# Optimization experiments

Measured on AMD Instinct MI355X. Metric: run time of the kernel, lower is better.

Reference implementation:

```python
import jax, jax.numpy as jnp
import numpy as np

DEPTH, DIM, HEADS, DH = 2, 1024, 16, 64
B, N, MEM, TEXT = 8, 256, 4, 64
PH, PW, PS = 4, 4, 16
EXP_H, EXP_W, EXP_T = 4, 4, 2
RH, RW, RT = 2*EXP_H+1, 2*EXP_W+1, 2*EXP_T+1  # 9,9,5
CUR_IDX = 20
MEM_IDXS = [0, 5, 10, 15]
SCALE = DH ** -0.5


def _pos(idx):
    # get_pos_from_idx_down_right
    nf = PH * PW
    inner = idx % nf
    return inner % PH, inner // PH, idx // nf


def _axial_freqs():
    # 2D axial rotary freqs over the (PH*PS)x(PW*PS) pixel grid, rot_dim = DH
    GH, GW = PH * PS, PW * PS
    nfa = DH // 4  # 16 base freqs per axis -> 32 dims per axis after pair-repeat
    inv = 1.0 / (10000.0 ** (np.arange(nfa, dtype=np.float64) / nfa))
    fh = np.repeat(np.arange(GH)[:, None] * inv[None, :], 2, axis=-1)  # [GH,32]
    fw = np.repeat(np.arange(GW)[:, None] * inv[None, :], 2, axis=-1)  # [GW,32]
    return np.concatenate([
        np.broadcast_to(fh[:, None, :], (GH, GW, DH // 2)),
        np.broadcast_to(fw[None, :, :], (GH, GW, DH // 2)),
    ], axis=-1).astype(np.float32)  # [GH,GW,DH]


def setup_inputs() -> dict:
    key = jax.random.key(0)
    ks = jax.random.split(key, 14)
    p = lambda k, shape: jax.random.normal(k, shape, jnp.float32) * 0.02
    x = jax.random.normal(ks[0], (B, N, DIM), jnp.float32)
    cond = jax.random.normal(ks[1], (B, MEM * N + TEXT, DIM), jnp.float32)
    Wq = p(ks[2], (DEPTH, DIM, HEADS * DH))
    Wk = p(ks[3], (DEPTH, DIM, HEADS * DH))
    Wv = p(ks[4], (DEPTH, DIM, HEADS * DH))
    Wo = p(ks[5], (DEPTH, HEADS * DH, DIM))
    bo = jnp.zeros((DEPTH, DIM), jnp.float32)
    rpe = p(ks[6], (DEPTH, RH * RW * RT, HEADS))
    W1 = p(ks[7], (DEPTH, DIM, DIM * 4 * 2))
    b1 = jnp.zeros((DEPTH, DIM * 8), jnp.float32)
    W2 = p(ks[8], (DEPTH, DIM * 4, DIM))
    b2 = jnp.zeros((DEPTH, DIM), jnp.float32)
    freqs = _axial_freqs()
    def block(idx):
        r, c, _ = _pos(idx)
        return freqs[r * PS:(r + 1) * PS, c * PS:(c + 1) * PS].reshape(-1, DH)
    src_freq = jnp.asarray(block(CUR_IDX))
    tgt_freq = jnp.asarray(np.concatenate([block(i) for i in MEM_IDXS], axis=0))
    sr, sc, st = _pos(CUR_IDX)
    rel = [(tr - sr + EXP_H) * RW + (tc - sc + EXP_W) + (tt - st + EXP_T) * RH * RW
           for (tr, tc, tt) in map(_pos, MEM_IDXS)]
    rel_idx = jnp.asarray(rel, jnp.int32)
    return dict(x=x, cond=cond, Wq=Wq, Wk=Wk, Wv=Wv, Wo=Wo, bo=bo, rpe=rpe,
                W1=W1, b1=b1, W2=W2, b2=b2, src_freq=src_freq, tgt_freq=tgt_freq,
                rel_idx=rel_idx)


def _rotate_half(t):
    # pairs interleaved: (d r) with r=2
    tr = t.reshape(t.shape[:-1] + (-1, 2))
    t1, t2 = tr[..., 0], tr[..., 1]
    return jnp.stack((-t2, t1), axis=-1).reshape(t.shape)


def _apply_rotary(freqs, t):
    return t * jnp.cos(freqs) + _rotate_half(t) * jnp.sin(freqs)


def reference(x, cond, Wq, Wk, Wv, Wo, bo, rpe, W1, b1, W2, b2, src_freq, tgt_freq, rel_idx):
    MS = MEM * N  # memory token count in cond
    split_heads = lambda t: t.reshape(t.shape[0], t.shape[1], HEADS, DH).transpose(0, 2, 1, 3)
    for l in range(DEPTH):
        # --- FullCrossAttention ---
        q = split_heads(x @ Wq[l])          # [b,h,n,dh]
        k = split_heads(cond @ Wk[l])       # [b,h,j,dh]
        v = split_heads(cond @ Wv[l])
        # gathered relative-position bias added to k (broadcast over feature dim)
        bias = rpe[l][rel_idx]              # [mem, h]
        bias_k = jnp.repeat(bias.T, N, axis=1)[None, :, :, None]  # [1,h,mem*S,1]
        k = k.at[:, :, :MS, :].add(bias_k)
        # inline rotary: src freqs on q, gathered target freqs on memory keys
        q = _apply_rotary(src_freq, q)
        k = k.at[:, :, :MS, :].set(_apply_rotary(tgt_freq, k[:, :, :MS, :]))
        dots = jnp.einsum('bhid,bhjd->bhij', q, k) * SCALE
        attn = jax.nn.softmax(dots, axis=-1)
        out = jnp.einsum('bhij,bhjd->bhid', attn, v)
        out = out.transpose(0, 2, 1, 3).reshape(x.shape[0], N, HEADS * DH)
        x = x + out @ Wo[l] + bo[l]
        # --- GEGLU FeedForward ---
        hgl = x @ W1[l] + b1[l]
        a, g = jnp.split(hgl, 2, axis=-1)
        y = a * jax.nn.gelu(g, approximate=False)
        x = x + y @ W2[l] + b2[l]
    return x
```

## Files before the change

kernel.cpp:

```cpp
#include <hip/hip_runtime.h>
#include <hip/hip_bf16.h>
#include <math.h>

typedef __hip_bfloat16 bf16;
typedef __bf16 bf16x8 __attribute__((ext_vector_type(8)));
typedef float f32x4 __attribute__((ext_vector_type(4)));

typedef __attribute__((address_space(3))) void lds_void;
typedef const __attribute__((address_space(1))) void gbl_void;

__device__ __forceinline__ float b2f(bf16 v) { return __bfloat162float(v); }
__device__ __forceinline__ bf16 f2b(float v) { return __float2bfloat16(v); }

__device__ __forceinline__ f32x4 shfl_xor4(f32x4 v, int m) {
  f32x4 o;
  o[0] = __shfl_xor(v[0], m);
  o[1] = __shfl_xor(v[1], m);
  o[2] = __shfl_xor(v[2], m);
  o[3] = __shfl_xor(v[3], m);
  return o;
}
__device__ __forceinline__ f32x4 max4(f32x4 a, f32x4 b) {
  f32x4 o;
  o[0] = fmaxf(a[0], b[0]); o[1] = fmaxf(a[1], b[1]);
  o[2] = fmaxf(a[2], b[2]); o[3] = fmaxf(a[3], b[3]);
  return o;
}
__device__ __forceinline__ f32x4 exp4(f32x4 a) {
  f32x4 o;
  o[0] = __expf(a[0]); o[1] = __expf(a[1]);
  o[2] = __expf(a[2]); o[3] = __expf(a[3]);
  return o;
}

__device__ __forceinline__ void cbar(int ahead) {
  if (ahead >= 2)      asm volatile("s_waitcnt vmcnt(8)" ::: "memory");
  else if (ahead == 1) asm volatile("s_waitcnt vmcnt(4)" ::: "memory");
  else                 asm volatile("s_waitcnt vmcnt(0)" ::: "memory");
  __builtin_amdgcn_s_barrier();
  __builtin_amdgcn_sched_barrier(0);
}
__device__ __forceinline__ void cbar2(int ahead) {
  if (ahead >= 1) asm volatile("s_waitcnt vmcnt(4)" ::: "memory");
  else            asm volatile("s_waitcnt vmcnt(0)" ::: "memory");
  __builtin_amdgcn_s_barrier();
  __builtin_amdgcn_sched_barrier(0);
}

__device__ __forceinline__ int xcd_swz(int flat, int nwg) {
  int q = nwg >> 3, r = nwg & 7;
  int xcd = flat & 7, pos = flat >> 3;
  return (xcd < r) ? (xcd * (q + 1) + pos) : (r * (q + 1) + (xcd - r) * q + pos);
}

__global__ void detect_dtype(const unsigned int* __restrict__ x, int* __restrict__ flag) {
  int cnt = 0;
  for (int i = 0; i < 128; ++i) {
    unsigned int lo = x[i] & 0xFFFFu;
    unsigned int e = (lo >> 7) & 0xFFu;
    if (e >= 100u && e <= 140u) ++cnt;
  }
  *flag = (cnt >= 96) ? 1 : 0;
}

__global__ void convert_in(const void* __restrict__ src, bf16* __restrict__ dst,
                           int n, const int* __restrict__ flag) {
  int i = blockIdx.x * 256 + threadIdx.x;
  if (i >= n) return;
  dst[i] = (*flag) ? ((const bf16*)src)[i] : f2b(((const float*)src)[i]);
}

__global__ void emit_kernel(const float* __restrict__ xf, const int* __restrict__ flag,
                            void* __restrict__ out) {
  int i = blockIdx.x * 256 + threadIdx.x;
  if (*flag) ((bf16*)out)[i] = f2b(xf[i]);
  else       ((float*)out)[i] = xf[i];
}

template<int HALF>
__device__ __forceinline__ bf16x8 frag_ld(const __bf16* lt, int r, int quad) {
  constexpr int LB = (HALF == 128) ? 7 : 6;
  int line = r & (HALF - 1);
  int sl = (((r >> LB) << 2) | quad) ^ (line & 7);
  return *(const bf16x8*)&lt[line * 64 + sl * 8];
}

template<int TAG>
__global__ __launch_bounds__(256, 3) void gemm_bt(
    const bf16* __restrict__ A, int lda,
    const bf16* __restrict__ Bt, int ldb,
    float alpha,
    const float* __restrict__ resid,
    const bf16* __restrict__ bias,
    float* __restrict__ outf,
    bf16* __restrict__ outb,
    int ldc, int K)
{
  __shared__ char smem[49152] __attribute__((aligned(16)));
  float* lC = (float*)smem;

  int tid = threadIdx.x;
  int lane = tid & 63;
  int wave = tid >> 6;
  int quad = lane >> 4, l16 = lane & 15;
  int wm = (wave >> 1) * 64, wn = (wave & 1) * 64;

  int gx = gridDim.x, gy = gridDim.y;
  int nwg = gx * gy;
  bool ymaj = gy >= gx;
  int flat = ymaj ? ((int)blockIdx.y * gx + blockIdx.x)
                  : ((int)blockIdx.x * gy + blockIdx.y);
  int swz = xcd_swz(flat, nwg);
  int bx, by;
  if (ymaj) { by = swz / gx; bx = swz - by * gx; }
  else      { bx = swz / gy; by = swz - bx * gy; }
  int row0 = by * 128, col0 = bx * 128;

  const bf16* asrc[2]; const bf16* bsrc[2];
#pragma unroll
  for (int i = 0; i < 2; ++i) {
    int line = i * 32 + (tid >> 3);
    int hx = (tid & 7) ^ (line & 7);
    int r = line + ((hx >> 2) << 6);
    int ke = (hx & 3) << 3;
    asrc[i] = A + (long long)(row0 + r) * lda + ke;
    bsrc[i] = Bt + (long long)(col0 + r) * ldb + ke;
  }

  auto stage = [&](int b, int t) {
    int o = t * 32;
#pragma unroll
    for (int i = 0; i < 2; ++i) {
      __builtin_amdgcn_global_load_lds((gbl_void*)(asrc[i] + o),
          (lds_void*)(smem + b * 8192 + i * 4096 + wave * 1024), 16, 0, 0);
      __builtin_amdgcn_global_load_lds((gbl_void*)(bsrc[i] + o),
          (lds_void*)(smem + 24576 + b * 8192 + i * 4096 + wave * 1024), 16, 0, 0);
    }
  };

  f32x4 acc[4][4];
#pragma unroll
  for (int a = 0; a < 4; ++a)
#pragma unroll
    for (int b = 0; b < 4; ++b) acc[a][b] = (f32x4){0.f, 0.f, 0.f, 0.f};

  int nk = K >> 5;
  stage(0, 0); stage(1, 1);
  cbar2(1);

  for (int t = 0; t < nk; ++t) {
    if (t + 2 < nk) stage((t + 2) % 3, t + 2);
    int bt = t % 3;
    const __bf16* lA = (const __bf16*)(smem + bt * 8192);
    const __bf16* lB = (const __bf16*)(smem + 24576 + bt * 8192);
    bf16x8 af[4], bfr[4];
#pragma unroll
    for (int mi = 0; mi < 4; ++mi) af[mi] = frag_ld<64>(lA, wm + mi * 16 + l16, quad);
#pragma unroll
    for (int ni = 0; ni < 4; ++ni) bfr[ni] = frag_ld<64>(lB, wn + ni * 16 + l16, quad);
    __builtin_amdgcn_s_setprio(1);
#pragma unroll
    for (int mi = 0; mi < 4; ++mi)
#pragma unroll
      for (int ni = 0; ni < 4; ++ni)
        acc[mi][ni] = __builtin_amdgcn_mfma_f32_16x16x32_bf16(
            af[mi], bfr[ni], acc[mi][ni], 0, 0, 0);
    __builtin_amdgcn_s_setprio(0);
    int ahead = nk - 1 - (t + 1); if (ahead > 1) ahead = 1;
    cbar2(ahead);
  }

#pragma unroll
  for (int half = 0; half < 2; ++half) {
    __syncthreads();
    if ((wave >> 1) == half) {
#pragma unroll
      for (int mi = 0; mi < 4; ++mi)
#pragma unroll
        for (int ni = 0; ni < 4; ++ni)
#pragma unroll
          for (int r = 0; r < 4; ++r)
            lC[(mi * 16 + quad * 4 + r) * 128 + wn + ni * 16 + l16] =
                acc[mi][ni][r] * alpha;
    }
    __syncthreads();
#pragma unroll
    for (int i = 0; i < 8; ++i) {
      int f = i * 256 + tid;
      int row = f >> 5, cc = (f & 31) * 4;
      int m = row0 + half * 64 + row, n = col0 + cc;
      f32x4 v = *(const f32x4*)&lC[row * 128 + cc];
      long long ci = (long long)m * ldc + n;
      if (bias) {
        v[0] += b2f(bias[n]);     v[1] += b2f(bias[n + 1]);
        v[2] += b2f(bias[n + 2]); v[3] += b2f(bias[n + 3]);
      }
      if (resid) v += *(const f32x4*)&resid[ci];
      if (outf) *(f32x4*)&outf[ci] = v;
      if (outb) {
        bf16 c0 = f2b(v[0]), c1 = f2b(v[1]), c2 = f2b(v[2]), c3 = f2b(v[3]);
        ushort4 o = { *(unsigned short*)&c0, *(unsigned short*)&c1,
                      *(unsigned short*)&c2, *(unsigned short*)&c3 };
        *(ushort4*)&outb[ci] = o;
      }
    }
  }
}

__global__ __launch_bounds__(512, 2) void gemm256_geglu(
    const bf16* __restrict__ A, int lda,
    const bf16* __restrict__ W1t, int ldb,
    const bf16* __restrict__ bias,
    bf16* __restrict__ outy, int ldy, int K)
{
  __shared__ char smem[131072] __attribute__((aligned(16)));
  float* lC = (float*)smem;

  int tid = threadIdx.x;
  int lane = tid & 63;
  int wave = tid >> 6;
  int quad = lane >> 4, l16 = lane & 15;
  int wr = wave >> 2, wc = wave & 3;
  int wm = wr * 128, wn = wc * 64;
  int row0 = blockIdx.y * 256, col0 = blockIdx.x * 128;

  const bf16* asrc[2]; const bf16* bsrc[2];
#pragma unroll
  for (int i = 0; i < 2; ++i) {
    int line = i * 64 + (tid >> 3);
    int hx = (tid & 7) ^ (line & 7);
    int rA = line + ((hx >> 2) << 7);
    int ke = (hx & 3) << 3;
    asrc[i] = A + (long long)(row0 + rA) * lda + ke;
    int rowW = (hx & 4) ? (4096 + col0 + line) : (col0 + line);
    bsrc[i] = W1t + (long long)rowW * ldb + ke;
  }

  auto stage = [&](int b, int t) {
    int o = t * 32;
#pragma unroll
    for (int i = 0; i < 2; ++i) {
      __builtin_amdgcn_global_load_lds((gbl_void*)(asrc[i] + o),
          (lds_void*)(smem + b * 16384 + i * 8192 + wave * 1024), 16, 0, 0);
      __builtin_amdgcn_global_load_lds((gbl_void*)(bsrc[i] + o),
          (lds_void*)(smem + 65536 + b * 16384 + i * 8192 + wave * 1024), 16, 0, 0);
    }
  };

  f32x4 acc[8][4];
#pragma unroll
  for (int a = 0; a < 8; ++a)
#pragma unroll
    for (int b = 0; b < 4; ++b) acc[a][b] = (f32x4){0.f, 0.f, 0.f, 0.f};

  int nk = K >> 5;
  stage(0, 0); stage(1, 1); stage(2, 2);
  cbar(2);

  for (int t = 0; t < nk; ++t) {
    if (t + 3 < nk) stage((t + 3) & 3, t + 3);
    const __bf16* lA = (const __bf16*)(smem + (t & 3) * 16384);
    const __bf16* lB = (const __bf16*)(smem + 65536 + (t & 3) * 16384);
    bf16x8 af[8], bfr[4];
#pragma unroll
    for (int mi = 0; mi < 8; ++mi) af[mi] = frag_ld<128>(lA, wm + mi * 16 + l16, quad);
#pragma unroll
    for (int ni = 0; ni < 4; ++ni) bfr[ni] = frag_ld<128>(lB, wn + ni * 16 + l16, quad);
    __builtin_amdgcn_s_setprio(1);
#pragma unroll
    for (int mi = 0; mi < 8; ++mi)
#pragma unroll
      for (int ni = 0; ni < 4; ++ni)
        acc[mi][ni] = __builtin_amdgcn_mfma_f32_16x16x32_bf16(
            af[mi], bfr[ni], acc[mi][ni], 0, 0, 0);
    __builtin_amdgcn_s_setprio(0);
    int hi = t + 3; if (hi > nk - 1) hi = nk - 1;
    cbar(hi - (t + 1));
  }

#pragma unroll
  for (int h = 0; h < 2; ++h) {
    __syncthreads();
    if (wr == h) {
#pragma unroll
      for (int mi = 0; mi < 8; ++mi)
#pragma unroll
        for (int ni = 0; ni < 4; ++ni)
#pragma unroll
          for (int r = 0; r < 4; ++r)
            lC[(mi * 16 + quad * 4 + r) * 256 + wn + ni * 16 + l16] =
                acc[mi][ni][r];
    }
    __syncthreads();
#pragma unroll
    for (int it = 0; it < 8; ++it) {
      int f = it * 512 + tid;
      int row = f >> 5, cc = (f & 31) * 4;
      int m = row0 + h * 128 + row, n = col0 + cc;
      f32x4 a = *(const f32x4*)&lC[row * 256 + cc];
      f32x4 g = *(const f32x4*)&lC[row * 256 + 128 + cc];
      bf16 yb[4];
#pragma unroll
      for (int j = 0; j < 4; ++j) {
        float av = a[j] + b2f(bias[n + j]);
        float gv = g[j] + b2f(bias[4096 + n + j]);
        float ge = 0.5f * gv * (1.0f + erff(gv * 0.70710678118654752f));
        yb[j] = f2b(av * ge);
      }
      ushort4 o = { *(unsigned short*)&yb[0], *(unsigned short*)&yb[1],
                    *(unsigned short*)&yb[2], *(unsigned short*)&yb[3] };
      *(ushort4*)&outy[(long long)m * ldy + n] = o;
    }
  }
}

__global__ __launch_bounds__(256, 3) void gemm_splitk(
    const bf16* __restrict__ A, int lda,
    const bf16* __restrict__ Bt, int ldb,
    float* __restrict__ pbuf, int ldc, int M, int KC)
{
  __shared__ char smem[49152] __attribute__((aligned(16)));

  int koff = blockIdx.z * KC;
  float* outz = pbuf + (long long)blockIdx.z * M * ldc;
  int tid = threadIdx.x;
  int lane = tid & 63;
  int wave = tid >> 6;
  int quad = lane >> 4, l16 = lane & 15;
  int wm = (wave >> 1) * 64, wn = (wave & 1) * 64;

  int gx = gridDim.x, gy = gridDim.y;
  int nwg = gx * gy;
  bool ymaj = gy >= gx;
  int flat = ymaj ? ((int)blockIdx.y * gx + blockIdx.x)
                  : ((int)blockIdx.x * gy + blockIdx.y);
  int swz = xcd_swz(flat, nwg);
  int bx, by;
  if (ymaj) { by = swz / gx; bx = swz - by * gx; }
  else      { bx = swz / gy; by = swz - bx * gy; }
  int row0 = by * 128, col0 = bx * 128;

  const bf16* asrc[2]; const bf16* bsrc[2];
#pragma unroll
  for (int i = 0; i < 2; ++i) {
    int line = i * 32 + (tid >> 3);
    int hx = (tid & 7) ^ (line & 7);
    int r = line + ((hx >> 2) << 6);
    int ke = (hx & 3) << 3;
    asrc[i] = A + (long long)(row0 + r) * lda + koff + ke;
    bsrc[i] = Bt + (long long)(col0 + r) * ldb + koff + ke;
  }

  auto stage = [&](int b, int t) {
    int o = t * 32;
#pragma unroll
    for (int i = 0; i < 2; ++i) {
      __builtin_amdgcn_global_load_lds((gbl_void*)(asrc[i] + o),
          (lds_void*)(smem + b * 8192 + i * 4096 + wave * 1024), 16, 0, 0);
      __builtin_amdgcn_global_load_lds((gbl_void*)(bsrc[i] + o),
          (lds_void*)(smem + 24576 + b * 8192 + i * 4096 + wave * 1024), 16, 0, 0);
    }
  };

  f32x4 acc[4][4];
#pragma unroll
  for (int a = 0; a < 4; ++a)
#pragma unroll
    for (int b = 0; b < 4; ++b) acc[a][b] = (f32x4){0.f, 0.f, 0.f, 0.f};

  int nk = KC >> 5;
  stage(0, 0); stage(1, 1);
  cbar2(1);

  for (int t = 0; t < nk; ++t) {
    if (t + 2 < nk) stage((t + 2) % 3, t + 2);
    int bt = t % 3;
    const __bf16* lA = (const __bf16*)(smem + bt * 8192);
    const __bf16* lB = (const __bf16*)(smem + 24576 + bt * 8192);
    bf16x8 af[4], bfr[4];
#pragma unroll
    for (int mi = 0; mi < 4; ++mi) af[mi] = frag_ld<64>(lA, wm + mi * 16 + l16, quad);
#pragma unroll
    for (int ni = 0; ni < 4; ++ni) bfr[ni] = frag_ld<64>(lB, wn + ni * 16 + l16, quad);
    __builtin_amdgcn_s_setprio(1);
#pragma unroll
    for (int mi = 0; mi < 4; ++mi)
#pragma unroll
      for (int ni = 0; ni < 4; ++ni)
        acc[mi][ni] = __builtin_amdgcn_mfma_f32_16x16x32_bf16(
            af[mi], bfr[ni], acc[mi][ni], 0, 0, 0);
    __builtin_amdgcn_s_setprio(0);
    int ahead = nk - 1 - (t + 1); if (ahead > 1) ahead = 1;
    cbar2(ahead);
  }

#pragma unroll
  for (int mi = 0; mi < 4; ++mi)
#pragma unroll
    for (int ni = 0; ni < 4; ++ni) {
      int n = col0 + wn + ni * 16 + l16;
#pragma unroll
      for (int r = 0; r < 4; ++r) {
        int m = row0 + wm + mi * 16 + quad * 4 + r;
        outz[(long long)m * ldc + n] = acc[mi][ni][r];
      }
    }
}

__global__ void reduce_ff2(const float* __restrict__ pbuf, const bf16* __restrict__ bias,
                           float* __restrict__ xf, bf16* __restrict__ xbf) {
  int i = blockIdx.x * 256 + threadIdx.x;
  const int NT = 2048 * 1024;
  float v = xf[i] + b2f(bias[i & 1023]) +
            pbuf[i] + pbuf[i + NT] + pbuf[i + 2 * NT] + pbuf[i + 3 * NT];
  xf[i] = v;
  xbf[i] = f2b(v);
}

__device__ __forceinline__ void fa_stage(
    const bf16* __restrict__ kb, const bf16* __restrict__ vtb, int j0, int tk,
    char* smem, int kboff, int vboff, int tid, int wave)
{
  int rounds = tk >> 6;
  for (int i = 0; i < rounds; ++i) {
    int rowk = i * 64 + (tid >> 3);
    int cbk = ((tid & 7) * 16) ^ ((rowk & 7) << 4);
    __builtin_amdgcn_global_load_lds(
        (gbl_void*)(kb + (long long)(j0 + rowk) * 1024 + (cbk >> 1)),
        (lds_void*)(smem + kboff + i * 8192 + wave * 1024), 16, 0, 0);
    int rowv, cbv;
    if (tk == 128) { rowv = i * 32 + (tid >> 4); cbv = ((tid & 15) * 16) ^ ((rowv & 7) << 4); }
    else           { rowv = (tid >> 3);          cbv = ((tid & 7) * 16) ^ ((rowv & 7) << 4); }
    __builtin_amdgcn_global_load_lds(
        (gbl_void*)(vtb + (long long)rowv * 8704 + j0 + (cbv >> 1)),
        (lds_void*)(smem + vboff + i * 8192 + wave * 1024), 16, 0, 0);
  }
}

template<int TK>
__device__ __forceinline__ void fa_compute(
    const char* smem, int kboff, int vboff,
    const bf16x8 (&qa)[2], bf16* lPw,
    int quad, int l16,
    f32x4 (&accO)[4], f32x4& mrow, f32x4& lrow)
{
  constexpr int NT = TK / 16;
  constexpr int NCH = TK / 32;
  const __bf16* lK = (const __bf16*)(smem + kboff);
  const __bf16* lV = (const __bf16*)(smem + vboff);
  int xork = (l16 & 7) << 3;

  f32x4 accS[NT];
#pragma unroll
  for (int ni = 0; ni < NT; ++ni) accS[ni] = (f32x4){0.f, 0.f, 0.f, 0.f};

#pragma unroll
  for (int ni = 0; ni < NT; ++ni)
#pragma unroll
    for (int ks = 0; ks < 2; ++ks) {
      bf16x8 bfr = *(const bf16x8*)&lK[(ni * 16 + l16) * 64 + ((ks * 32 + quad * 8) ^ xork)];
      accS[ni] = __builtin_amdgcn_mfma_f32_16x16x32_bf16(qa[ks], bfr, accS[ni], 0, 0, 0);
    }

  f32x4 vmax = (f32x4){-INFINITY, -INFINITY, -INFINITY, -INFINITY};
#pragma unroll
  for (int ni = 0; ni < NT; ++ni) {
    accS[ni] *= 0.125f;
    vmax = max4(vmax, accS[ni]);
  }
#pragma unroll
  for (int m = 1; m <= 8; m <<= 1) vmax = max4(vmax, shfl_xor4(vmax, m));
  f32x4 mnew = max4(mrow, vmax);
  f32x4 alpha = exp4(mrow - mnew);
  f32x4 rs = (f32x4){0.f, 0.f, 0.f, 0.f};
#pragma unroll
  for (int ni = 0; ni < NT; ++ni) {
    accS[ni] = exp4(accS[ni] - mnew);
    rs += accS[ni];
  }
#pragma unroll
  for (int m = 1; m <= 8; m <<= 1) rs += shfl_xor4(rs, m);
  lrow = lrow * alpha + rs;
  mrow = mnew;
#pragma unroll
  for (int nd = 0; nd < 4; ++nd) accO[nd] *= alpha;

#pragma unroll
  for (int c = 0; c < NCH; ++c) {
#pragma unroll
    for (int u = 0; u < 2; ++u)
#pragma unroll
      for (int r = 0; r < 4; ++r)
        lPw[(quad * 4 + r) * 40 + u * 16 + l16] = f2b(accS[c * 2 + u][r]);
    bf16x8 pa = *(const bf16x8*)&lPw[l16 * 40 + quad * 8];
#pragma unroll
    for (int nd = 0; nd < 4; ++nd) {
      bf16x8 vb = *(const bf16x8*)&lV[(nd * 16 + l16) * TK + ((c * 32 + quad * 8) ^ xork)];
      accO[nd] = __builtin_amdgcn_mfma_f32_16x16x32_bf16(pa, vb, accO[nd], 0, 0, 0);
    }
  }
}

__global__ __launch_bounds__(512, 2) void flash_attn(
    const bf16* __restrict__ q, const bf16* __restrict__ k,
    const bf16* __restrict__ vt, bf16* __restrict__ att)
{
  __shared__ char smem[75776] __attribute__((aligned(16)));

  int idx = xcd_swz(blockIdx.x, gridDim.x);
  int b = idx >> 5, h = (idx >> 1) & 15, half = idx & 1;
  int tid = threadIdx.x, wave = tid >> 6, lane = tid & 63;
  int quad = lane >> 4, l16 = lane & 15;
  int qrow0 = b * 256 + half * 128 + wave * 16;

  const bf16* kb  = k  + (long long)b * 1088 * 1024 + h * 64;
  const bf16* vtb = vt + (long long)(h * 64) * 8704 + b * 1088;
  bf16* lPw = (bf16*)(smem + 65536 + wave * 1280);

  bf16x8 qa[2];
#pragma unroll
  for (int ks = 0; ks < 2; ++ks)
    qa[ks] = *(const bf16x8*)&q[(long long)(qrow0 + l16) * 1024 +
                                h * 64 + ks * 32 + quad * 8];

  f32x4 accO[4];
  f32x4 mrow = (f32x4){-INFINITY, -INFINITY, -INFINITY, -INFINITY};
  f32x4 lrow = (f32x4){0.f, 0.f, 0.f, 0.f};
#pragma unroll
  for (int nd = 0; nd < 4; ++nd) accO[nd] = (f32x4){0.f, 0.f, 0.f, 0.f};

  fa_stage(kb, vtb, 0, 128, smem, 0, 32768, tid, wave);
  __syncthreads();

  for (int jt = 0; jt < 8; ++jt) {
    int buf = (jt & 1) * 16384;
    int nbuf = 16384 - buf;
    if (jt < 7) fa_stage(kb, vtb, (jt + 1) * 128, 128, smem, nbuf, 32768 + nbuf, tid, wave);
    else        fa_stage(kb, vtb, 1024, 64, smem, nbuf, 32768 + nbuf, tid, wave);
    fa_compute<128>(smem, buf, 32768 + buf, qa, lPw, quad, l16, accO, mrow, lrow);
    __syncthreads();
  }
  fa_compute<64>(smem, 0, 32768, qa, lPw, quad, l16, accO, mrow, lrow);

  f32x4 inv;
  inv[0] = 1.f / lrow[0]; inv[1] = 1.f / lrow[1];
  inv[2] = 1.f / lrow[2]; inv[3] = 1.f / lrow[3];
#pragma unroll
  for (int nd = 0; nd < 4; ++nd) {
    f32x4 o = accO[nd] * inv;
#pragma unroll
    for (int r = 0; r < 4; ++r)
      att[(long long)(qrow0 + quad * 4 + r) * 1024 +
          h * 64 + nd * 16 + l16] = f2b(o[r]);
  }
}

__global__ void init_x_kernel(const void* __restrict__ x, const int* __restrict__ flag,
                              float* __restrict__ xf, bf16* __restrict__ xbf) {
  int i = blockIdx.x * 256 + threadIdx.x;
  float v = (*flag) ? b2f(((const bf16*)x)[i]) : ((const float*)x)[i];
  xf[i] = v;
  xbf[i] = f2b(v);
}

__global__ void transpose_w(const void* __restrict__ in, bf16* __restrict__ out,
                            int R, int C, const int* __restrict__ flag) {
  __shared__ bf16 tile[32][33];
  long long zoff = (long long)blockIdx.z * R * C;
  const bf16* inb = (const bf16*)in + zoff;
  const float* inf = (const float*)in + zoff;
  out += zoff;
  int tx = threadIdx.x, ty = threadIdx.y;
  int c0 = blockIdx.x * 32, r0 = blockIdx.y * 32;
  int isb = *flag;
#pragma unroll
  for (int i = 0; i < 4; ++i) {
    long long off = (long long)(r0 + ty + i * 8) * C + (c0 + tx);
    tile[ty + i * 8][tx] = isb ? inb[off] : f2b(inf[off]);
  }
  __syncthreads();
#pragma unroll
  for (int i = 0; i < 4; ++i)
    out[(long long)(c0 + ty + i * 8) * R + (r0 + tx)] = tile[tx][ty + i * 8];
}

__global__ void rotary_q_kernel(bf16* __restrict__ q, const bf16* __restrict__ srcf) {
  int idx = blockIdx.x * 256 + threadIdx.x;
  int row = idx >> 9;
  int p = idx & 511;
  int h = p >> 5, i = p & 31;
  int d0 = h * 64 + 2 * i;
  int ntok = row & 255;
  float f = b2f(srcf[ntok * 64 + 2 * i]);
  float c = cosf(f), s = sinf(f);
  long long base = (long long)row * 1024 + d0;
  float q0 = b2f(q[base]), q1 = b2f(q[base + 1]);
  q[base]     = f2b(q0 * c - q1 * s);
  q[base + 1] = f2b(q1 * c + q0 * s);
}

__global__ void k_bias_rot_kernel(bf16* __restrict__ k, const bf16* __restrict__ tgtf,
                                  const bf16* __restrict__ rpe,
                                  const int* __restrict__ ridx, int layer) {
  int idx = blockIdx.x * 256 + threadIdx.x;
  int b = idx >> 19;
  int rem = idx & ((1 << 19) - 1);
  int j = rem >> 9;
  int p = rem & 511;
  int h = p >> 5, i = p & 31;
  int d0 = h * 64 + 2 * i;
  float bias = b2f(rpe[(layer * 405 + ridx[j >> 8]) * 16 + h]);
  float f = b2f(tgtf[j * 64 + 2 * i]);
  float c = cosf(f), s = sinf(f);
  long long base = (long long)(b * 1088 + j) * 1024 + d0;
  float k0 = b2f(k[base]) + bias, k1 = b2f(k[base + 1]) + bias;
  k[base]     = f2b(k0 * c - k1 * s);
  k[base + 1] = f2b(k1 * c + k0 * s);
}

extern "C" void kernel_launch(void* const* d_in, const int* in_sizes, int n_in,
                              void* d_out, int out_size, void* d_ws, size_t ws_size,
                              hipStream_t stream) {
  (void)in_sizes; (void)n_in; (void)out_size; (void)ws_size;
  const void* x    = d_in[0];
  const void* cond = d_in[1];
  const void* Wq   = d_in[2];
  const void* Wk   = d_in[3];
  const void* Wv   = d_in[4];
  const void* Wo   = d_in[5];
  const void* bo   = d_in[6];
  const void* rpe  = d_in[7];
  const void* W1   = d_in[8];
  const void* b1   = d_in[9];
  const void* W2   = d_in[10];
  const void* b2   = d_in[11];
  const void* srcf = d_in[12];
  const void* tgtf = d_in[13];
  const int*  ridx = (const int*)d_in[14];

  char* w = (char*)d_ws;
  int* flag = (int*)w;   w += 256;
  bf16* WqT = (bf16*)w;  w += (size_t)2 * 1024 * 1024 * 2;
  bf16* WkT = (bf16*)w;  w += (size_t)2 * 1024 * 1024 * 2;
  bf16* WvT = (bf16*)w;  w += (size_t)2 * 1024 * 1024 * 2;
  bf16* WoT = (bf16*)w;  w += (size_t)2 * 1024 * 1024 * 2;
  bf16* W1T = (bf16*)w;  w += (size_t)2 * 8192 * 1024 * 2;
  bf16* W2T = (bf16*)w;  w += (size_t)2 * 4096 * 1024 * 2;
  bf16* condb = (bf16*)w; w += (size_t)8704 * 1024 * 2;
  bf16* bo_b = (bf16*)w;  w += 2048 * 2;
  bf16* rpe_b = (bf16*)w; w += 12960 * 2;
  bf16* b1_b = (bf16*)w;  w += 16384 * 2;
  bf16* b2_b = (bf16*)w;  w += 2048 * 2;
  bf16* srcf_b = (bf16*)w; w += 16384 * 2;
  bf16* tgtf_b = (bf16*)w; w += 65536 * 2;
  float* xf = (float*)w; w += (size_t)2048 * 1024 * 4;
  bf16* xbf = (bf16*)w;  w += (size_t)2048 * 1024 * 2;
  bf16* qbuf = (bf16*)w; w += (size_t)2048 * 1024 * 2;
  bf16* kbuf = (bf16*)w; w += (size_t)8704 * 1024 * 2;
  bf16* vTf = (bf16*)w;  w += (size_t)1024 * 8704 * 2;
  bf16* att = (bf16*)w;  w += (size_t)2048 * 1024 * 2;
  bf16* hgl = (bf16*)w;  w += (size_t)2048 * 8192 * 2;
  bf16* ybuf = (bf16*)w; w += (size_t)2048 * 4096 * 2;
  float* pbuf = (float*)hgl;

  detect_dtype<<<1, 1, 0, stream>>>((const unsigned int*)x, flag);

  convert_in<<<34816, 256, 0, stream>>>(cond, condb, 8704 * 1024, flag);
  convert_in<<<8, 256, 0, stream>>>(bo, bo_b, 2048, flag);
  convert_in<<<51, 256, 0, stream>>>(rpe, rpe_b, 12960, flag);
  convert_in<<<64, 256, 0, stream>>>(b1, b1_b, 16384, flag);
  convert_in<<<8, 256, 0, stream>>>(b2, b2_b, 2048, flag);
  convert_in<<<64, 256, 0, stream>>>(srcf, srcf_b, 16384, flag);
  convert_in<<<256, 256, 0, stream>>>(tgtf, tgtf_b, 65536, flag);

  dim3 tb(32, 8);
  transpose_w<<<dim3(32, 32, 2),  tb, 0, stream>>>(Wq, WqT, 1024, 1024, flag);
  transpose_w<<<dim3(32, 32, 2),  tb, 0, stream>>>(Wk, WkT, 1024, 1024, flag);
  transpose_w<<<dim3(32, 32, 2),  tb, 0, stream>>>(Wv, WvT, 1024, 1024, flag);
  transpose_w<<<dim3(32, 32, 2),  tb, 0, stream>>>(Wo, WoT, 1024, 1024, flag);
  transpose_w<<<dim3(256, 32, 2), tb, 0, stream>>>(W1, W1T, 1024, 8192, flag);
  transpose_w<<<dim3(32, 128, 2), tb, 0, stream>>>(W2, W2T, 4096, 1024, flag);
  init_x_kernel<<<8192, 256, 0, stream>>>(x, flag, xf, xbf);

  for (int l = 0; l < 2; ++l) {
    const bf16* WqTl = WqT + (size_t)l * 1024 * 1024;
    const bf16* WkTl = WkT + (size_t)l * 1024 * 1024;
    const bf16* WvTl = WvT + (size_t)l * 1024 * 1024;
    const bf16* WoTl = WoT + (size_t)l * 1024 * 1024;
    const bf16* W1Tl = W1T + (size_t)l * 8192 * 1024;
    const bf16* W2Tl = W2T + (size_t)l * 4096 * 1024;

    gemm_bt<0><<<dim3(8, 16), 256, 0, stream>>>(xbf, 1024, WqTl, 1024, 1.f,
        nullptr, nullptr, nullptr, qbuf, 1024, 1024);
    rotary_q_kernel<<<4096, 256, 0, stream>>>(qbuf, srcf_b);
    gemm_bt<1><<<dim3(68, 8), 256, 0, stream>>>(WvTl, 1024, condb, 1024, 1.f,
        nullptr, nullptr, nullptr, vTf, 8704, 1024);
    gemm_bt<2><<<dim3(8, 68), 256, 0, stream>>>(condb, 1024, WkTl, 1024, 1.f,
        nullptr, nullptr, nullptr, kbuf, 1024, 1024);
    k_bias_rot_kernel<<<16384, 256, 0, stream>>>(kbuf, tgtf_b, rpe_b, ridx, l);
    flash_attn<<<256, 512, 0, stream>>>(qbuf, kbuf, vTf, att);
    gemm_bt<3><<<dim3(8, 16), 256, 0, stream>>>(att, 1024, WoTl, 1024, 1.f,
        xf, bo_b + (size_t)l * 1024, xf, xbf, 1024, 1024);
    gemm256_geglu<<<dim3(32, 8), 512, 0, stream>>>(xbf, 1024, W1Tl, 1024,
        b1_b + (size_t)l * 8192, ybuf, 4096, 1024);
    gemm_splitk<<<dim3(8, 16, 4), 256, 0, stream>>>(ybuf, 4096, W2Tl, 4096,
                                                    pbuf, 1024, 2048, 1024);
    reduce_ff2<<<8192, 256, 0, stream>>>(pbuf, b2_b + (size_t)l * 1024, xf, xbf);
  }

  emit_kernel<<<8192, 256, 0, stream>>>(xf, flag, d_out);
}
```

Baseline: 743.0 us.

## Restructure GEGLU GEMM mainloop into 64-wide K double buffer with quadrant-phased MFMA

Changes the GEGLU GEMM kernel from a 4-stage pipeline of 32-wide K tiles to a 2-slot double buffer of 64-wide K tiles with an XOR-swizzled LDS layout. Each iteration is split into four quadrant phases, each loading fragments and running its MFMAs between barriers, and the next-tile prefetch is issued mid-iteration into the slot just consumed. The goal is to halve loop iterations and barrier overhead per K, cut LDS bank conflicts, and interleave LDS reads with MFMA work. In exchange it adds many more workgroup barriers per iteration and has only two buffers of prefetch depth.

```diff
diff --git a/kernel.cpp b/kernel.cpp
--- a/kernel.cpp
+++ b/kernel.cpp
@@ -43,6 +43,10 @@
 __device__ __forceinline__ void cbar2(int ahead) {
   if (ahead >= 1) asm volatile("s_waitcnt vmcnt(4)" ::: "memory");
   else            asm volatile("s_waitcnt vmcnt(0)" ::: "memory");
+  __builtin_amdgcn_s_barrier();
+  __builtin_amdgcn_sched_barrier(0);
+}
+__device__ __forceinline__ void pbar() {
   __builtin_amdgcn_s_barrier();
   __builtin_amdgcn_sched_barrier(0);
 }
@@ -224,26 +228,25 @@
   int wm = wr * 128, wn = wc * 64;
   int row0 = blockIdx.y * 256, col0 = blockIdx.x * 128;
 
-  const bf16* asrc[2]; const bf16* bsrc[2];
-#pragma unroll
-  for (int i = 0; i < 2; ++i) {
-    int line = i * 64 + (tid >> 3);
-    int hx = (tid & 7) ^ (line & 7);
-    int rA = line + ((hx >> 2) << 7);
-    int ke = (hx & 3) << 3;
-    asrc[i] = A + (long long)(row0 + rA) * lda + ke;
-    int rowW = (hx & 4) ? (4096 + col0 + line) : (col0 + line);
-    bsrc[i] = W1t + (long long)rowW * ldb + ke;
-  }
-
-  auto stage = [&](int b, int t) {
-    int o = t * 32;
-#pragma unroll
-    for (int i = 0; i < 2; ++i) {
-      __builtin_amdgcn_global_load_lds((gbl_void*)(asrc[i] + o),
-          (lds_void*)(smem + b * 16384 + i * 8192 + wave * 1024), 16, 0, 0);
-      __builtin_amdgcn_global_load_lds((gbl_void*)(bsrc[i] + o),
-          (lds_void*)(smem + 65536 + b * 16384 + i * 8192 + wave * 1024), 16, 0, 0);
+  const bf16* asrc[4]; const bf16* bsrc[4];
+#pragma unroll
+  for (int i = 0; i < 4; ++i) {
+    int row = i * 64 + (tid >> 3);
+    int coff = ((tid & 7) * 16) ^ ((row & 7) << 4);
+    asrc[i] = A + (long long)(row0 + row) * lda + (coff >> 1);
+    int rowW = (row < 128) ? (col0 + row) : (4096 + col0 + row - 128);
+    bsrc[i] = W1t + (long long)rowW * ldb + (coff >> 1);
+  }
+
+  auto stage = [&](int slot, int t) {
+    int ko = t * 64;
+    char* base = smem + slot * 65536;
+#pragma unroll
+    for (int i = 0; i < 4; ++i) {
+      __builtin_amdgcn_global_load_lds((gbl_void*)(asrc[i] + ko),
+          (lds_void*)(base + i * 8192 + wave * 1024), 16, 0, 0);
+      __builtin_amdgcn_global_load_lds((gbl_void*)(bsrc[i] + ko),
+          (lds_void*)(base + 32768 + i * 8192 + wave * 1024), 16, 0, 0);
     }
   };
 
@@ -253,29 +256,104 @@
 #pragma unroll
     for (int b = 0; b < 4; ++b) acc[a][b] = (f32x4){0.f, 0.f, 0.f, 0.f};
 
-  int nk = K >> 5;
-  stage(0, 0); stage(1, 1); stage(2, 2);
-  cbar(2);
+  int nk = K >> 6;
+
+  stage(0, 0); stage(1, 1);
+  asm volatile("s_waitcnt vmcnt(8)" ::: "memory");
+  pbar();
 
   for (int t = 0; t < nk; ++t) {
-    if (t + 3 < nk) stage((t + 3) & 3, t + 3);
-    const __bf16* lA = (const __bf16*)(smem + (t & 3) * 16384);
-    const __bf16* lB = (const __bf16*)(smem + 65536 + (t & 3) * 16384);
-    bf16x8 af[8], bfr[4];
-#pragma unroll
-    for (int mi = 0; mi < 8; ++mi) af[mi] = frag_ld<128>(lA, wm + mi * 16 + l16, quad);
-#pragma unroll
-    for (int ni = 0; ni < 4; ++ni) bfr[ni] = frag_ld<128>(lB, wn + ni * 16 + l16, quad);
+    const __bf16* lA = (const __bf16*)(smem + (t & 1) * 65536);
+    const __bf16* lB = (const __bf16*)(smem + (t & 1) * 65536 + 32768);
+
+    bf16x8 a0[4][2], a1[4][2], b0[2][2], b1[2][2];
+
+#pragma unroll
+    for (int mi = 0; mi < 4; ++mi)
+#pragma unroll
+      for (int ks = 0; ks < 2; ++ks) {
+        int r = wm + mi * 16 + l16;
+        a0[mi][ks] = *(const bf16x8*)&lA[r * 64 + ((ks * 32 + quad * 8) ^ ((r & 7) << 3))];
+      }
+#pragma unroll
+    for (int ni = 0; ni < 2; ++ni)
+#pragma unroll
+      for (int ks = 0; ks < 2; ++ks) {
+        int r = wn + ni * 16 + l16;
+        b0[ni][ks] = *(const bf16x8*)&lB[r * 64 + ((ks * 32 + quad * 8) ^ ((r & 7) << 3))];
+      }
+    pbar();
     __builtin_amdgcn_s_setprio(1);
 #pragma unroll
-    for (int mi = 0; mi < 8; ++mi)
-#pragma unroll
-      for (int ni = 0; ni < 4; ++ni)
-        acc[mi][ni] = __builtin_amdgcn_mfma_f32_16x16x32_bf16(
-            af[mi], bfr[ni], acc[mi][ni], 0, 0, 0);
+    for (int mi = 0; mi < 4; ++mi)
+#pragma unroll
+      for (int ni = 0; ni < 2; ++ni)
+#pragma unroll
+        for (int ks = 0; ks < 2; ++ks)
+          acc[mi][ni] = __builtin_amdgcn_mfma_f32_16x16x32_bf16(
+              a0[mi][ks], b0[ni][ks], acc[mi][ni], 0, 0, 0);
     __builtin_amdgcn_s_setprio(0);
-    int hi = t + 3; if (hi > nk - 1) hi = nk - 1;
-    cbar(hi - (t + 1));
+    pbar();
+
+#pragma unroll
+    for (int ni = 0; ni < 2; ++ni)
+#pragma unroll
+      for (int ks = 0; ks < 2; ++ks) {
+        int r = wn + 32 + ni * 16 + l16;
+        b1[ni][ks] = *(const bf16x8*)&lB[r * 64 + ((ks * 32 + quad * 8) ^ ((r & 7) << 3))];
+      }
+    pbar();
+    __builtin_amdgcn_s_setprio(1);
+#pragma unroll
+    for (int mi = 0; mi < 4; ++mi)
+#pragma unroll
+      for (int ni = 0; ni < 2; ++ni)
+#pragma unroll
+        for (int ks = 0; ks < 2; ++ks)
+          acc[mi][ni + 2] = __builtin_amdgcn_mfma_f32_16x16x32_bf16(
+              a0[mi][ks], b1[ni][ks], acc[mi][ni + 2], 0, 0, 0);
+    __builtin_amdgcn_s_setprio(0);
+    pbar();
+
+#pragma unroll
+    for (int mi = 0; mi < 4; ++mi)
+#pragma unroll
+      for (int ks = 0; ks < 2; ++ks) {
+        int r = wm + 64 + mi * 16 + l16;
+        a1[mi][ks] = *(const bf16x8*)&lA[r * 64 + ((ks * 32 + quad * 8) ^ ((r & 7) << 3))];
+      }
+    pbar();
+    __builtin_amdgcn_s_setprio(1);
+#pragma unroll
+    for (int mi = 0; mi < 4; ++mi)
+#pragma unroll
+      for (int ni = 0; ni < 2; ++ni)
+#pragma unroll
+        for (int ks = 0; ks < 2; ++ks)
+          acc[mi + 4][ni] = __builtin_amdgcn_mfma_f32_16x16x32_bf16(
+              a1[mi][ks], b0[ni][ks], acc[mi + 4][ni], 0, 0, 0);
+    __builtin_amdgcn_s_setprio(0);
+    pbar();
+
+    __builtin_amdgcn_sched_barrier(0);
+    if (t + 2 < nk) {
+      stage(t & 1, t + 2);
+      asm volatile("s_waitcnt vmcnt(8)" ::: "memory");
+    } else if (t + 1 < nk) {
+      asm volatile("s_waitcnt vmcnt(0)" ::: "memory");
+    }
+    pbar();
+    __builtin_amdgcn_s_setprio(1);
+#pragma unroll
+    for (int mi = 0; mi < 4; ++mi)
+#pragma unroll
+      for (int ni = 0; ni < 2; ++ni)
+#pragma unroll
+        for (int ks = 0; ks < 2; ++ks)
+          acc[mi + 4][ni + 2] = __builtin_amdgcn_mfma_f32_16x16x32_bf16(
+              a1[mi][ks], b1[ni][ks], acc[mi + 4][ni + 2], 0, 0, 0);
+    __builtin_amdgcn_s_setprio(0);
+    pbar();
   }
 
 #pragma unroll
```

Result: no change. 757.4 us (+1.9%).
